# Kernel optimization log

Measured on AMD Instinct MI355X. Metric: run time of the kernel, lower is better.

The kernel has to match this reference:

```python
import math
import jax, jax.numpy as jnp
import numpy as np

N_LAYER = 6
THETA = 2.0 ** 16
LN_EPS = 1e-5


def _ln(x):
    # LayerNorm over last dim, no affine (elementwise_affine=False)
    mu = x.mean(-1, keepdims=True)
    var = ((x - mu) ** 2).mean(-1, keepdims=True)
    return (x - mu) / jnp.sqrt(var + LN_EPS)


def _rope(phases, v):
    # phases: (T, N); v: (B, H, T, N)
    ph = (phases % 1.0) * (2.0 * math.pi)
    c, s = jnp.cos(ph), jnp.sin(ph)
    v2 = v.reshape(v.shape[:-1] + (-1, 2))
    v_rot = jnp.stack((-v2[..., 1], v2[..., 0]), axis=-1).reshape(v.shape)
    return v * c + v_rot * s


def setup_inputs() -> dict:
    key = jax.random.key(0)
    ks = jax.random.split(key, 6)
    B, T, D, nh, mult, V = 2, 512, 256, 4, 64, 256
    N = D * mult // nh  # 4096 neurons per head
    std = 0.02
    return {
        "input_ids": jax.random.randint(ks[0], (B, T), 0, V, dtype=jnp.int64),
        "embed_table": jax.random.normal(ks[1], (V, D), jnp.float32) * std,
        "encoder": jax.random.normal(ks[2], (nh, D, N), jnp.float32) * std,
        "encoder_v": jax.random.normal(ks[3], (nh, D, N), jnp.float32) * std,
        "decoder": jax.random.normal(ks[4], (nh * N, D), jnp.float32) * std,
        "lm_head": jax.random.normal(ks[5], (D, V), jnp.float32) * std,
    }


def reference(input_ids, embed_table, encoder, encoder_v, decoder, lm_head):
    B, T = input_ids.shape
    nh, D, N = encoder.shape
    # RoPE freqs: quantize(arange(N), 2) / N exponent (matches get_freqs)
    qidx = jnp.floor(jnp.arange(N, dtype=jnp.float32) / 2.0) * 2.0
    freqs = 1.0 / (THETA ** (qidx / N)) / (2.0 * math.pi)
    phases = jnp.arange(T, dtype=jnp.float32)[:, None] * freqs[None, :]  # (T, N)
    # strictly-lower causal mask (tril with diagonal=-1)
    causal = jnp.tril(jnp.ones((T, T), dtype=bool), k=-1)
    dec = decoder.reshape(nh, N, D)  # head-major, matches transpose(1,2).reshape

    x = _ln(embed_table[input_ids])[:, None]  # (B, 1, T, D)
    trace = None
    for _ in range(N_LAYER):  # shared (tied) weights across layers
        x_sparse = jax.nn.relu(jnp.einsum('bitd,hdn->bhtn', x, encoder))  # (B,H,T,N)
        qr = _rope(phases, x_sparse)
        scores = jnp.einsum('bhtn,bhsn->bhts', qr, qr)  # linear attn, no softmax
        scores = jnp.where(causal, scores, 0.0)
        ykv = _ln(jnp.einsum('bhts,bisd->bhtd', scores, x))  # (B,H,T,D)
        y_sparse = jax.nn.relu(jnp.einsum('bhtd,hdn->bhtn', ykv, encoder_v))
        xy_sparse = x_sparse * y_sparse  # elementwise gate
        trace = xy_sparse  # keep only last layer (used for neuron_trace)
        ymlp = jnp.einsum('bhtn,hnd->btd', xy_sparse, dec)[:, None]  # (B,1,T,D)
        x = _ln(x + _ln(ymlp))

    xs = x[:, 0]  # (B, T, D)
    logits = xs @ lm_head  # (B, T, V)
    embedding = xs.mean(axis=1)  # (B, D), pool_output, no mask
    neuron_trace = trace.mean(axis=2).reshape(B, -1)  # (B, H*N)
    return logits, embedding, neuron_trace
```

## Files before the change

### kernel.cpp

```cpp
#include <hip/hip_runtime.h>
#include <hip/hip_bf16.h>

#define TT 512
#define DD 256
#define NH 4
#define NN 4096
#define VV 256
#define NLAYER 6
#define BB 2
#define BH (BB * NH)
#define NPAIR 2048

typedef __attribute__((ext_vector_type(8))) short bf16x8;
typedef __attribute__((ext_vector_type(4))) float f32x4;
typedef __attribute__((ext_vector_type(8))) unsigned short us8;
typedef __attribute__((ext_vector_type(4))) unsigned short us4;

#define AS1 __attribute__((address_space(1)))
#define AS3 __attribute__((address_space(3)))

__device__ __forceinline__ void glds16(const unsigned short* g, unsigned short* l) {
  __builtin_amdgcn_global_load_lds((const AS1 void*)g, (AS3 void*)l, 16, 0, 0);
}

__device__ __forceinline__ unsigned short f2bf(float f) {
  unsigned int u = __float_as_uint(f);
  return (unsigned short)((u + 0x7FFFu + ((u >> 16) & 1u)) >> 16);
}
__device__ __forceinline__ float bf2f(unsigned short h) {
  return __uint_as_float((unsigned int)h << 16);
}

__device__ __forceinline__ float block_sum_256(float v) {
  __shared__ float s[4];
  #pragma unroll
  for (int o = 32; o > 0; o >>= 1) v += __shfl_down(v, o);
  int lane = threadIdx.x & 63, wid = threadIdx.x >> 6;
  if (lane == 0) s[wid] = v;
  __syncthreads();
  float r = s[0] + s[1] + s[2] + s[3];
  __syncthreads();
  return r;
}

__device__ __forceinline__ float wave_sum64(float v) {
  #pragma unroll
  for (int o = 32; o > 0; o >>= 1) v += __shfl_xor(v, o);
  return v;
}

__device__ __forceinline__ void mfma_tile128_glds(const unsigned short* __restrict__ A, int lda,
                                                  const unsigned short* __restrict__ B, int ldb,
                                                  int K, f32x4 acc[4][4],
                                                  unsigned short* As, unsigned short* Bs) {
  const int tid = threadIdx.x;
  const int lane = tid & 63, wave = tid >> 6;
  const int fm = lane & 15, fq = lane >> 4;
  const int rw = (wave >> 1) << 6, cw = (wave & 1) << 6;
  const int lrow = lane >> 3;
  const int scol = (((lane & 7) ^ lrow) << 3);
  const unsigned short* gA = A + (size_t)(wave * 8 + lrow) * lda + scol;
  const unsigned short* gB = B + (size_t)(wave * 8 + lrow) * ldb + scol;
  unsigned short* lA = As + wave * 8 * 64;
  unsigned short* lB = Bs + wave * 8 * 64;
  const int swz = (fm & 7) << 4;
  for (int k0 = 0; k0 < K; k0 += 64) {
    __syncthreads();
    #pragma unroll
    for (int i = 0; i < 4; ++i) {
      glds16(gA + k0 + (size_t)(i * 32) * lda, lA + i * 32 * 64);
      glds16(gB + k0 + (size_t)(i * 32) * ldb, lB + i * 32 * 64);
    }
    __syncthreads();
    #pragma unroll
    for (int kk = 0; kk < 2; ++kk) {
      bf16x8 af[4], bfv[4];
      #pragma unroll
      for (int i = 0; i < 4; ++i) {
        const int ra = rw + i * 16 + fm;
        const int rb = cw + i * 16 + fm;
        af[i]  = *(const bf16x8*)((const char*)As + ((((ra << 7) + (kk << 6) + (fq << 4))) ^ swz));
        bfv[i] = *(const bf16x8*)((const char*)Bs + ((((rb << 7) + (kk << 6) + (fq << 4))) ^ swz));
      }
      #pragma unroll
      for (int mi = 0; mi < 4; ++mi)
        #pragma unroll
        for (int ni = 0; ni < 4; ++ni)
          acc[mi][ni] = __builtin_amdgcn_mfma_f32_16x16x32_bf16(af[mi], bfv[ni], acc[mi][ni], 0, 0, 0);
    }
  }
}


__global__ __launch_bounds__(256) void k_csinit(float2* __restrict__ cs) {
  int idx = blockIdx.x * 256 + threadIdx.x;
  int t = idx >> 11, p = idx & (NPAIR - 1);
  const float INV2PI = 0.15915494309189535f;
  const float TWOPI = 6.283185307179586f;
  float f = exp2f(-16.0f * (float)(2 * p) / (float)NN) * INV2PI;
  float ph = fmodf((float)t * f, 1.0f) * TWOPI;
  float s, c;
  sincosf(ph, &s, &c);
  cs[idx] = make_float2(c, s);
}

__global__ __launch_bounds__(256) void k_tcast(const float* __restrict__ in,
                                               unsigned short* __restrict__ out,
                                               int R, int C) {
  __shared__ float tile[64][65];
  const size_t zoff = (size_t)blockIdx.z * R * C;
  const int r0 = blockIdx.y * 64, c0 = blockIdx.x * 64;
  const int cl = threadIdx.x & 63, r4 = threadIdx.x >> 6;
  #pragma unroll 4
  for (int i = 0; i < 16; ++i) {
    int rl = r4 * 16 + i;
    tile[rl][cl] = in[zoff + (size_t)(r0 + rl) * C + c0 + cl];
  }
  __syncthreads();
  #pragma unroll 4
  for (int i = 0; i < 16; ++i) {
    int ccl = r4 * 16 + i;
    out[zoff + (size_t)(c0 + ccl) * R + r0 + cl] = f2bf(tile[cl][ccl]);
  }
}

__global__ __launch_bounds__(256) void k_embed_ln(const int* __restrict__ idw,
                                                  const float* __restrict__ tbl,
                                                  float* __restrict__ x,
                                                  unsigned short* __restrict__ xbf,
                                                  unsigned short* __restrict__ xTbf) {
  __shared__ int s_id;
  int row = blockIdx.x, tid = threadIdx.x;
  if (tid == 0) {
    bool is64 = true;
    for (int i = 1; i < 64; i += 2)
      if (idw[i] != 0) { is64 = false; break; }
    s_id = is64 ? idw[2 * row] : idw[row];
  }
  __syncthreads();
  int id = s_id;
  float v = tbl[(size_t)id * DD + tid];
  float mu = block_sum_256(v) * (1.0f / DD);
  float d = v - mu;
  float var = block_sum_256(d * d) * (1.0f / DD);
  float r = d * rsqrtf(var + 1e-5f);
  x[(size_t)row * DD + tid] = r;
  unsigned short rb = f2bf(r);
  xbf[(size_t)row * DD + tid] = rb;
  int b = row >> 9, t = row & 511;
  xTbf[((size_t)b * DD + tid) * TT + t] = rb;
}


__global__ __launch_bounds__(256) void k_enc(const unsigned short* __restrict__ xbf,
                                             const unsigned short* __restrict__ encT,
                                             const float2* __restrict__ cs,
                                             unsigned short* __restrict__ xsp,
                                             unsigned short* __restrict__ qr) {
  __shared__ float smemf[8192];
  unsigned short* As = (unsigned short*)smemf;
  unsigned short* Bs = As + 8192;
  float (*Sc)[132] = (float(*)[132])smemf;
  const int tid = threadIdx.x;
  const int lin = blockIdx.x;
  const int bh = lin & 7, r0 = lin >> 3;
  const int b = bh >> 2, h = bh & 3;
  const int m0 = (r0 >> 5) * 128, n0 = (r0 & 31) * 128;
  f32x4 acc[4][4] = {};
  mfma_tile128_glds(xbf + (size_t)b * TT * DD + (size_t)m0 * DD, DD,
                    encT + (size_t)h * NN * DD + (size_t)n0 * DD, DD, DD, acc, As, Bs);
  const int lane = tid & 63, wave = tid >> 6;
  const int fm = lane & 15, fq = lane >> 4;
  const int cw = (wave & 1) << 6;
  const int rbase = ((wave >> 1) << 4) + (fq << 2);
  const size_t base = (size_t)bh * TT * NN;
  const int rr = tid >> 3, cc = (tid & 7) << 4;
  #pragma unroll
  for (int mi = 0; mi < 4; ++mi) {
    __syncthreads();
    #pragma unroll
    for (int ni = 0; ni < 4; ++ni)
      #pragma unroll
      for (int r = 0; r < 4; ++r)
        Sc[rbase + r][cw + ni * 16 + fm] = acc[mi][ni][r];
    __syncthreads();
    float v[16];
    *(float4*)&v[0]  = *(const float4*)&Sc[rr][cc];
    *(float4*)&v[4]  = *(const float4*)&Sc[rr][cc + 4];
    *(float4*)&v[8]  = *(const float4*)&Sc[rr][cc + 8];
    *(float4*)&v[12] = *(const float4*)&Sc[rr][cc + 12];
    const int t = m0 + ((rr >> 4) << 6) + mi * 16 + (rr & 15);
    const int n = n0 + cc;
    #pragma unroll
    for (int j = 0; j < 16; ++j) v[j] = fmaxf(v[j], 0.0f);
    us8 o0, o1;
    #pragma unroll
    for (int j = 0; j < 8; ++j) { o0[j] = f2bf(v[j]); o1[j] = f2bf(v[8 + j]); }
    size_t off = base + (size_t)t * NN + n;
    *(us8*)(xsp + off) = o0;
    *(us8*)(xsp + off + 8) = o1;
    float cv[16];
    const float* cp = (const float*)(cs + (size_t)t * NPAIR + (n >> 1));
    *(float4*)&cv[0]  = *(const float4*)(cp);
    *(float4*)&cv[4]  = *(const float4*)(cp + 4);
    *(float4*)&cv[8]  = *(const float4*)(cp + 8);
    *(float4*)&cv[12] = *(const float4*)(cp + 12);
    us8 q0, q1;
    #pragma unroll
    for (int j = 0; j < 8; ++j) {
      float c = cv[2 * j], s = cv[2 * j + 1];
      float ve = v[2 * j], vo = v[2 * j + 1];
      float qe = ve * c - vo * s;
      float qo = vo * c + ve * s;
      if (j < 4) { q0[2 * j] = f2bf(qe); q0[2 * j + 1] = f2bf(qo); }
      else       { q1[2 * (j - 4)] = f2bf(qe); q1[2 * (j - 4) + 1] = f2bf(qo); }
    }
    *(us8*)(qr + off) = q0;
    *(us8*)(qr + off + 8) = q1;
  }
}

__global__ __launch_bounds__(256) void k_scores_part(const unsigned short* __restrict__ qr,
                                                     float* __restrict__ scp) {
  __shared__ float smemf[8192];
  unsigned short* As = (unsigned short*)smemf;
  unsigned short* Bs = As + 8192;
  const int lin = blockIdx.x;
  const int xcd = lin & 7, slot = lin >> 3;
  const int zg = slot / 10, p = slot - zg * 10;
  const int z = xcd + 8 * zg;
  const int bh = z >> 2, kc = z & 3;
  const int mt = (p > 0) + (p > 2) + (p > 5);
  const int nt = p - mt * (mt + 1) / 2;
  const int m0 = mt * 128, n0 = nt * 128;
  const unsigned short* Q = qr + (size_t)bh * TT * NN + kc * 1024;
  f32x4 acc[4][4] = {};
  mfma_tile128_glds(Q + (size_t)m0 * NN, NN, Q + (size_t)n0 * NN, NN, 1024, acc, As, Bs);
  const int lane = threadIdx.x & 63, wave = threadIdx.x >> 6;
  const int fm = lane & 15, fq = lane >> 4;
  const int rw = (wave >> 1) << 6, cw = (wave & 1) << 6;
  float* C = scp + (size_t)z * TT * TT;
  #pragma unroll
  for (int ni = 0; ni < 4; ++ni) {
    int s = n0 + cw + ni * 16 + fm;
    #pragma unroll
    for (int mi = 0; mi < 4; ++mi) {
      int trow = m0 + rw + mi * 16 + (fq << 2);
      #pragma unroll
      for (int r = 0; r < 4; ++r)
        C[(size_t)(trow + r) * TT + s] = acc[mi][ni][r];
    }
  }
}

__global__ __launch_bounds__(256) void k_ykv_part(const float* __restrict__ scp,
                                                  const unsigned short* __restrict__ xTbf,
                                                  float* __restrict__ ykvp) {
  __shared__ unsigned short As[64][40];
  __shared__ unsigned short Bs[256][40];
  const int tid = threadIdx.x;
  const int lin = blockIdx.x;
  const int bh = lin & 7, r0 = lin >> 3;
  const int m0 = (r0 & 7) * 64, ks = r0 >> 3, b = bh >> 2;
  if (ks * 128 >= m0 + 64) return;
  float* C = ykvp + ((size_t)(bh * 4 + ks) * TT + m0) * DD;
  const int lane = tid & 63, wave = tid >> 6;
  const int srow = tid >> 2, sk = (tid & 3) << 3;
  const int fm = lane & 15, fq = lane >> 4;
  const int t = m0 + srow;
  const size_t abase0 = (size_t)(bh * 4) * TT * TT + (size_t)t * TT;
  const unsigned short* Brow = xTbf + ((size_t)b * DD + tid) * TT + ks * 128;
  f32x4 acc[16] = {};
  for (int k0 = 0; k0 < 128; k0 += 32) {
    us8 av;
    const int s0 = ks * 128 + k0 + sk;
    if (s0 >= t) {
      #pragma unroll
      for (int j = 0; j < 8; ++j) av[j] = 0;
    } else {
      const float* p = scp + abase0 + s0;
      float sum[8];
      #pragma unroll
      for (int j = 0; j < 8; ++j) sum[j] = 0.0f;
      #pragma unroll
      for (int kc = 0; kc < 4; ++kc) {
        float4 u0 = *(const float4*)(p + (size_t)kc * TT * TT);
        float4 u1 = *(const float4*)(p + (size_t)kc * TT * TT + 4);
        sum[0] += u0.x; sum[1] += u0.y; sum[2] += u0.z; sum[3] += u0.w;
        sum[4] += u1.x; sum[5] += u1.y; sum[6] += u1.z; sum[7] += u1.w;
      }
      #pragma unroll
      for (int j = 0; j < 8; ++j)
        av[j] = f2bf((s0 + j < t) ? sum[j] : 0.0f);
    }
    us8 bv0 = *(const us8*)(Brow + k0);
    us8 bv1 = *(const us8*)(Brow + k0 + 8);
    us8 bv2 = *(const us8*)(Brow + k0 + 16);
    us8 bv3 = *(const us8*)(Brow + k0 + 24);
    __syncthreads();
    *(us8*)(&As[srow][sk]) = av;
    *(us8*)(&Bs[tid][0]) = bv0;
    *(us8*)(&Bs[tid][8]) = bv1;
    *(us8*)(&Bs[tid][16]) = bv2;
    *(us8*)(&Bs[tid][24]) = bv3;
    __syncthreads();
    bf16x8 a = *(const bf16x8*)(&As[wave * 16 + fm][fq << 3]);
    #pragma unroll
    for (int ni = 0; ni < 16; ++ni) {
      bf16x8 bfr = *(const bf16x8*)(&Bs[ni * 16 + fm][fq << 3]);
      acc[ni] = __builtin_amdgcn_mfma_f32_16x16x32_bf16(a, bfr, acc[ni], 0, 0, 0);
    }
  }
  const int trow = wave * 16 + (fq << 2);
  #pragma unroll
  for (int ni = 0; ni < 16; ++ni)
    #pragma unroll
    for (int r = 0; r < 4; ++r)
      C[(size_t)(trow + r) * DD + ni * 16 + fm] = acc[ni][r];
}

__global__ __launch_bounds__(256) void k_ykv_red(const float* __restrict__ ykvp,
                                                 unsigned short* __restrict__ ykvbf) {
  int row = blockIdx.x * 4 + (threadIdx.x >> 6);
  int lane = threadIdx.x & 63;
  int bh = row >> 9, t = row & 511;
  int d0 = lane << 2;
  int nks = (t >> 7) + 1;
  size_t base = ((size_t)(bh * 4) * TT + t) * DD + d0;
  f32x4 v = *(const f32x4*)(ykvp + base);
  if (nks > 1) v += *(const f32x4*)(ykvp + base + (size_t)TT * DD);
  if (nks > 2) v += *(const f32x4*)(ykvp + base + (size_t)2 * TT * DD);
  if (nks > 3) v += *(const f32x4*)(ykvp + base + (size_t)3 * TT * DD);
  float mu = wave_sum64(v.x + v.y + v.z + v.w) * (1.0f / DD);
  f32x4 d = v - mu;
  float var = wave_sum64(d.x * d.x + d.y * d.y + d.z * d.z + d.w * d.w) * (1.0f / DD);
  f32x4 r = d * rsqrtf(var + 1e-5f);
  us4 rb;
  #pragma unroll
  for (int j = 0; j < 4; ++j) rb[j] = f2bf(r[j]);
  *(us4*)(ykvbf + (size_t)row * DD + d0) = rb;
}

__global__ __launch_bounds__(256) void k_ysp_xy(const unsigned short* __restrict__ ykvbf,
                                                const unsigned short* __restrict__ encvT,
                                                const unsigned short* __restrict__ xsp,
                                                unsigned short* __restrict__ xy) {
  __shared__ float smemf[8192];
  unsigned short* As = (unsigned short*)smemf;
  unsigned short* Bs = As + 8192;
  float (*Sc)[132] = (float(*)[132])smemf;
  const int tid = threadIdx.x;
  const int lin = blockIdx.x;
  const int bh = lin & 7, r0 = lin >> 3;
  const int h = bh & 3;
  const int m0 = (r0 >> 5) * 128, n0 = (r0 & 31) * 128;
  f32x4 acc[4][4] = {};
  mfma_tile128_glds(ykvbf + (size_t)bh * TT * DD + (size_t)m0 * DD, DD,
                    encvT + (size_t)h * NN * DD + (size_t)n0 * DD, DD, DD, acc, As, Bs);
  const int lane = tid & 63, wave = tid >> 6;
  const int fm = lane & 15, fq = lane >> 4;
  const int cw = (wave & 1) << 6;
  const int rbase = ((wave >> 1) << 4) + (fq << 2);
  const size_t base = (size_t)bh * TT * NN;
  const int rr = tid >> 3, cc = (tid & 7) << 4;
  #pragma unroll
  for (int mi = 0; mi < 4; ++mi) {
    __syncthreads();
    #pragma unroll
    for (int ni = 0; ni < 4; ++ni)
      #pragma unroll
      for (int r = 0; r < 4; ++r)
        Sc[rbase + r][cw + ni * 16 + fm] = acc[mi][ni][r];
    __syncthreads();
    float v[16];
    *(float4*)&v[0]  = *(const float4*)&Sc[rr][cc];
    *(float4*)&v[4]  = *(const float4*)&Sc[rr][cc + 4];
    *(float4*)&v[8]  = *(const float4*)&Sc[rr][cc + 8];
    *(float4*)&v[12] = *(const float4*)&Sc[rr][cc + 12];
    const int t = m0 + ((rr >> 4) << 6) + mi * 16 + (rr & 15);
    const int n = n0 + cc;
    size_t off = base + (size_t)t * NN + n;
    us8 x0 = *(const us8*)(xsp + off);
    us8 x1 = *(const us8*)(xsp + off + 8);
    us8 o0, o1;
    #pragma unroll
    for (int j = 0; j < 8; ++j) {
      o0[j] = f2bf(bf2f(x0[j]) * fmaxf(v[j], 0.0f));
      o1[j] = f2bf(bf2f(x1[j]) * fmaxf(v[8 + j], 0.0f));
    }
    *(us8*)(xy + off) = o0;
    *(us8*)(xy + off + 8) = o1;
  }
}

__global__ __launch_bounds__(256) void k_ymlp(const unsigned short* __restrict__ xy,
                                              const unsigned short* __restrict__ decT,
                                              float* __restrict__ ym32) {
  __shared__ float smemf[8192];
  unsigned short* As = (unsigned short*)smemf;
  unsigned short* Bs = As + 8192;
  const int lin = blockIdx.x;
  const int xcd = lin & 7, r0 = lin >> 3;
  const int z = xcd + 8 * (r0 >> 3);
  const int tile = r0 & 7;
  const int bh = z >> 3, ks = z & 7, h = bh & 3;
  const int m0 = (tile & 3) * 128, n0 = (tile >> 2) * 128;
  f32x4 acc[4][4] = {};
  mfma_tile128_glds(xy + (size_t)bh * TT * NN + (size_t)m0 * NN + ks * 512, NN,
                    decT + (size_t)h * DD * NN + (size_t)n0 * NN + ks * 512, NN,
                    512, acc, As, Bs);
  const int lane = threadIdx.x & 63, wave = threadIdx.x >> 6;
  const int fm = lane & 15, fq = lane >> 4;
  const int rw = (wave >> 1) << 6, cw = (wave & 1) << 6;
  float* C = ym32 + (size_t)z * TT * DD;
  #pragma unroll
  for (int ni = 0; ni < 4; ++ni) {
    int d = n0 + cw + ni * 16 + fm;
    #pragma unroll
    for (int mi = 0; mi < 4; ++mi) {
      int trow = m0 + rw + mi * 16 + (fq << 2);
      #pragma unroll
      for (int r = 0; r < 4; ++r)
        C[(size_t)(trow + r) * DD + d] = acc[mi][ni][r];
    }
  }
}

__global__ __launch_bounds__(256) void k_ln2(float* __restrict__ x,
                                             const float* __restrict__ ym32,
                                             unsigned short* __restrict__ xbf,
                                             unsigned short* __restrict__ xTbf) {
  int row = blockIdx.x * 4 + (threadIdx.x >> 6);
  int lane = threadIdx.x & 63;
  int b = row >> 9, t = row & 511;
  int d0 = lane << 2;
  f32x4 y = {0.0f, 0.0f, 0.0f, 0.0f};
  size_t rbase = (size_t)t * DD + d0;
  #pragma unroll
  for (int p = 0; p < 32; ++p)
    y += *(const f32x4*)(ym32 + (size_t)(b * 32 + p) * TT * DD + rbase);
  float mu = wave_sum64(y.x + y.y + y.z + y.w) * (1.0f / DD);
  f32x4 d = y - mu;
  float var = wave_sum64(d.x * d.x + d.y * d.y + d.z * d.z + d.w * d.w) * (1.0f / DD);
  f32x4 ly = d * rsqrtf(var + 1e-5f);
  f32x4 xv = *(const f32x4*)(x + (size_t)row * DD + d0) + ly;
  float mu2 = wave_sum64(xv.x + xv.y + xv.z + xv.w) * (1.0f / DD);
  f32x4 d2 = xv - mu2;
  float var2 = wave_sum64(d2.x * d2.x + d2.y * d2.y + d2.z * d2.z + d2.w * d2.w) * (1.0f / DD);
  f32x4 r = d2 * rsqrtf(var2 + 1e-5f);
  *(f32x4*)(x + (size_t)row * DD + d0) = r;
  us4 rb;
  #pragma unroll
  for (int j = 0; j < 4; ++j) rb[j] = f2bf(r[j]);
  *(us4*)(xbf + (size_t)row * DD + d0) = rb;
  #pragma unroll
  for (int j = 0; j < 4; ++j)
    xTbf[((size_t)b * DD + d0 + j) * TT + t] = rb[j];
}

__global__ __launch_bounds__(256) void k_trace_part(const unsigned short* __restrict__ xy,
                                                    float* __restrict__ part) {
  const int lin = blockIdx.x;
  const int ts = lin & 7, nc = (lin >> 3) & 1, bh = lin >> 4;
  const int n0 = nc * 2048 + threadIdx.x * 8;
  const size_t base = (size_t)bh * TT * NN + n0;
  float acc[8];
  #pragma unroll
  for (int j = 0; j < 8; ++j) acc[j] = 0.0f;
  for (int t = ts * 64; t < ts * 64 + 64; ++t) {
    us8 v = *(const us8*)(xy + base + (size_t)t * NN);
    #pragma unroll
    for (int j = 0; j < 8; ++j) acc[j] += bf2f(v[j]);
  }
  float* o = part + (size_t)(bh * 8 + ts) * NN + n0;
  #pragma unroll
  for (int j = 0; j < 8; ++j) o[j] = acc[j];
}

__global__ __launch_bounds__(256) void k_trace_red(const float* __restrict__ part,
                                                   float* __restrict__ out) {
  int idx = blockIdx.x * 256 + threadIdx.x;
  int bh = idx >> 12, n = idx & 4095;
  float s = 0.0f;
  #pragma unroll
  for (int ts = 0; ts < 8; ++ts)
    s += part[(size_t)(bh * 8 + ts) * NN + n];
  out[idx] = s * (1.0f / TT);
}

__global__ __launch_bounds__(256) void k_logits(const float* __restrict__ x,
                                                const float* __restrict__ W,
                                                float* __restrict__ out) {
  __shared__ float xs[DD];
  int row = blockIdx.x, tid = threadIdx.x;
  xs[tid] = x[(size_t)row * DD + tid];
  __syncthreads();
  float s = 0.0f;
  #pragma unroll 8
  for (int d = 0; d < DD; ++d) s = fmaf(xs[d], W[(size_t)d * VV + tid], s);
  out[(size_t)row * VV + tid] = s;
}

__global__ __launch_bounds__(256) void k_embedding(const float* __restrict__ x,
                                                   float* __restrict__ out) {
  int idx = blockIdx.x * 256 + threadIdx.x;
  int b = idx >> 8, d = idx & 255;
  float s = 0.0f;
  for (int t = 0; t < TT; ++t) s += x[(size_t)(b * TT + t) * DD + d];
  out[idx] = s * (1.0f / TT);
}

extern "C" void kernel_launch(void* const* d_in, const int* in_sizes, int n_in,
                              void* d_out, int out_size, void* d_ws, size_t ws_size,
                              hipStream_t stream) {
  const int*   ids  = (const int*)d_in[0];
  const float* tbl  = (const float*)d_in[1];
  const float* enc  = (const float*)d_in[2];
  const float* encv = (const float*)d_in[3];
  const float* dec  = (const float*)d_in[4];
  const float* lmh  = (const float*)d_in[5];

  float* ws   = (float*)d_ws;
  float* x    = ws;
  unsigned short* ykvbf = (unsigned short*)(x + 262144);
  float* ym32 = (float*)(ykvbf + 1048576);
  unsigned short* xbf   = (unsigned short*)(ym32 + 8388608);
  unsigned short* xTbf  = xbf + 262144;
  unsigned short* encT  = xTbf + 262144;
  unsigned short* encvT = encT + 4194304;
  unsigned short* decT  = encvT + 4194304;
  unsigned short* xspbf = decT + 4194304;
  unsigned short* qxybf = xspbf + 16777216;
  float2* cs  = (float2*)(qxybf + 16777216);
  float* scp  = (float*)(cs + 1048576);
  float* ykvp = scp + 8388608;

  float* out_logits = (float*)d_out;
  float* out_embed  = out_logits + (size_t)BB * TT * VV;
  float* out_trace  = out_embed + (size_t)BB * DD;

  k_csinit<<<(TT * NPAIR) / 256, 256, 0, stream>>>(cs);
  k_tcast<<<dim3(NN / 64, DD / 64, NH), 256, 0, stream>>>(enc,  encT,  DD, NN);
  k_tcast<<<dim3(NN / 64, DD / 64, NH), 256, 0, stream>>>(encv, encvT, DD, NN);
  k_tcast<<<dim3(DD / 64, NN / 64, NH), 256, 0, stream>>>(dec,  decT,  NN, DD);

  k_embed_ln<<<BB * TT, 256, 0, stream>>>(ids, tbl, x, xbf, xTbf);
  for (int l = 0; l < NLAYER; ++l) {
    k_enc        <<<1024, 256, 0, stream>>>(xbf, encT, cs, xspbf, qxybf);
    k_scores_part<<<320, 256, 0, stream>>>(qxybf, scp);
    k_ykv_part   <<<256, 256, 0, stream>>>(scp, xTbf, ykvp);
    k_ykv_red    <<<BH * TT / 4, 256, 0, stream>>>(ykvp, ykvbf);
    k_ysp_xy     <<<1024, 256, 0, stream>>>(ykvbf, encvT, xspbf, qxybf);
    k_ymlp       <<<512, 256, 0, stream>>>(qxybf, decT, ym32);
    k_ln2        <<<BB * TT / 4, 256, 0, stream>>>(x, ym32, xbf, xTbf);
  }
  k_trace_part<<<128, 256, 0, stream>>>(qxybf, scp);
  k_trace_red <<<128, 256, 0, stream>>>(scp, out_trace);
  k_logits    <<<BB * TT, 256, 0, stream>>>(x, lmh, out_logits);
  k_embedding <<<(BB * DD) / 256, 256, 0, stream>>>(x, out_embed);
}
```

Measured before the change: 816.4 us.

## Use BK=128 GEMM tile helper and move causal masking into scores epilogue

Adds a 128x128 MFMA tile routine that stages a 128-wide K slab per iteration with an XOR swizzle, halving the barrier/load rounds, and uses it in the scores and ymlp kernels (LDS doubled to 64KB per block). The scores kernel now zeroes the upper triangle on diagonal tiles so the ykv kernel can drop its per-element causal branch and mask. The larger LDS footprint may reduce occupancy, and ykv now reads unmasked partial buffers for off-diagonal regions that may be unwritten.

```diff
diff --git a/kernel.cpp b/kernel.cpp
--- a/kernel.cpp
+++ b/kernel.cpp
@@ -81,6 +81,45 @@
         const int rb = cw + i * 16 + fm;
         af[i]  = *(const bf16x8*)((const char*)As + ((((ra << 7) + (kk << 6) + (fq << 4))) ^ swz));
         bfv[i] = *(const bf16x8*)((const char*)Bs + ((((rb << 7) + (kk << 6) + (fq << 4))) ^ swz));
+      }
+      #pragma unroll
+      for (int mi = 0; mi < 4; ++mi)
+        #pragma unroll
+        for (int ni = 0; ni < 4; ++ni)
+          acc[mi][ni] = __builtin_amdgcn_mfma_f32_16x16x32_bf16(af[mi], bfv[ni], acc[mi][ni], 0, 0, 0);
+    }
+  }
+}
+
+__device__ __forceinline__ void mfma_tile128_bk128(const unsigned short* __restrict__ A, int lda,
+                                                   const unsigned short* __restrict__ B, int ldb,
+                                                   int K, f32x4 acc[4][4],
+                                                   unsigned short* As, unsigned short* Bs) {
+  const int tid = threadIdx.x;
+  const int lane = tid & 63, wave = tid >> 6;
+  const int fm = lane & 15, fq = lane >> 4;
+  const int rw = (wave >> 1) << 6, cw = (wave & 1) << 6;
+  const int lrow = lane >> 4;
+  const int cslot = lane & 15;
+  for (int k0 = 0; k0 < K; k0 += 128) {
+    __syncthreads();
+    #pragma unroll
+    for (int i = 0; i < 8; ++i) {
+      const int row = wave * 32 + i * 4 + lrow;
+      const int sc = (cslot ^ (row & 15)) << 3;
+      glds16(A + (size_t)row * lda + k0 + sc, As + (size_t)(wave * 32 + i * 4) * 128);
+      glds16(B + (size_t)row * ldb + k0 + sc, Bs + (size_t)(wave * 32 + i * 4) * 128);
+    }
+    __syncthreads();
+    #pragma unroll
+    for (int kk = 0; kk < 4; ++kk) {
+      bf16x8 af[4], bfv[4];
+      #pragma unroll
+      for (int i = 0; i < 4; ++i) {
+        const int ra = rw + i * 16 + fm;
+        const int rb = cw + i * 16 + fm;
+        af[i]  = *(const bf16x8*)((const char*)As + (((ra << 8) + (kk << 6) + (fq << 4)) ^ ((ra & 15) << 4)));
+        bfv[i] = *(const bf16x8*)((const char*)Bs + (((rb << 8) + (kk << 6) + (fq << 4)) ^ ((rb & 15) << 4)));
       }
       #pragma unroll
       for (int mi = 0; mi < 4; ++mi)
@@ -222,9 +261,9 @@
 
 __global__ __launch_bounds__(256) void k_scores_part(const unsigned short* __restrict__ qr,
                                                      float* __restrict__ scp) {
-  __shared__ float smemf[8192];
+  __shared__ float smemf[16384];
   unsigned short* As = (unsigned short*)smemf;
-  unsigned short* Bs = As + 8192;
+  unsigned short* Bs = As + 16384;
   const int lin = blockIdx.x;
   const int xcd = lin & 7, slot = lin >> 3;
   const int zg = slot / 10, p = slot - zg * 10;
@@ -235,11 +274,12 @@
   const int m0 = mt * 128, n0 = nt * 128;
   const unsigned short* Q = qr + (size_t)bh * TT * NN + kc * 1024;
   f32x4 acc[4][4] = {};
-  mfma_tile128_glds(Q + (size_t)m0 * NN, NN, Q + (size_t)n0 * NN, NN, 1024, acc, As, Bs);
+  mfma_tile128_bk128(Q + (size_t)m0 * NN, NN, Q + (size_t)n0 * NN, NN, 1024, acc, As, Bs);
   const int lane = threadIdx.x & 63, wave = threadIdx.x >> 6;
   const int fm = lane & 15, fq = lane >> 4;
   const int rw = (wave >> 1) << 6, cw = (wave & 1) << 6;
   float* C = scp + (size_t)z * TT * TT;
+  const bool diag = (m0 == n0);
   #pragma unroll
   for (int ni = 0; ni < 4; ++ni) {
     int s = n0 + cw + ni * 16 + fm;
@@ -247,8 +287,11 @@
     for (int mi = 0; mi < 4; ++mi) {
       int trow = m0 + rw + mi * 16 + (fq << 2);
       #pragma unroll
-      for (int r = 0; r < 4; ++r)
-        C[(size_t)(trow + r) * TT + s] = acc[mi][ni][r];
+      for (int r = 0; r < 4; ++r) {
+        float v = acc[mi][ni][r];
+        if (diag && s >= trow + r) v = 0.0f;
+        C[(size_t)(trow + r) * TT + s] = v;
+      }
     }
   }
 }
@@ -272,27 +315,23 @@
   const unsigned short* Brow = xTbf + ((size_t)b * DD + tid) * TT + ks * 128;
   f32x4 acc[16] = {};
   for (int k0 = 0; k0 < 128; k0 += 32) {
+    const int s0 = ks * 128 + k0 + sk;
+    const float* p = scp + abase0 + s0;
+    float sum[8];
+    float4 u0 = *(const float4*)(p);
+    float4 u1 = *(const float4*)(p + 4);
+    sum[0] = u0.x; sum[1] = u0.y; sum[2] = u0.z; sum[3] = u0.w;
+    sum[4] = u1.x; sum[5] = u1.y; sum[6] = u1.z; sum[7] = u1.w;
+    #pragma unroll
+    for (int kc = 1; kc < 4; ++kc) {
+      float4 v0 = *(const float4*)(p + (size_t)kc * TT * TT);
+      float4 v1 = *(const float4*)(p + (size_t)kc * TT * TT + 4);
+      sum[0] += v0.x; sum[1] += v0.y; sum[2] += v0.z; sum[3] += v0.w;
+      sum[4] += v1.x; sum[5] += v1.y; sum[6] += v1.z; sum[7] += v1.w;
+    }
     us8 av;
-    const int s0 = ks * 128 + k0 + sk;
-    if (s0 >= t) {
-      #pragma unroll
-      for (int j = 0; j < 8; ++j) av[j] = 0;
-    } else {
-      const float* p = scp + abase0 + s0;
-      float sum[8];
-      #pragma unroll
-      for (int j = 0; j < 8; ++j) sum[j] = 0.0f;
-      #pragma unroll
-      for (int kc = 0; kc < 4; ++kc) {
-        float4 u0 = *(const float4*)(p + (size_t)kc * TT * TT);
-        float4 u1 = *(const float4*)(p + (size_t)kc * TT * TT + 4);
-        sum[0] += u0.x; sum[1] += u0.y; sum[2] += u0.z; sum[3] += u0.w;
-        sum[4] += u1.x; sum[5] += u1.y; sum[6] += u1.z; sum[7] += u1.w;
-      }
-      #pragma unroll
-      for (int j = 0; j < 8; ++j)
-        av[j] = f2bf((s0 + j < t) ? sum[j] : 0.0f);
-    }
+    #pragma unroll
+    for (int j = 0; j < 8; ++j) av[j] = f2bf(sum[j]);
     us8 bv0 = *(const us8*)(Brow + k0);
     us8 bv1 = *(const us8*)(Brow + k0 + 8);
     us8 bv2 = *(const us8*)(Brow + k0 + 16);
@@ -396,9 +435,9 @@
 __global__ __launch_bounds__(256) void k_ymlp(const unsigned short* __restrict__ xy,
                                               const unsigned short* __restrict__ decT,
                                               float* __restrict__ ym32) {
-  __shared__ float smemf[8192];
+  __shared__ float smemf[16384];
   unsigned short* As = (unsigned short*)smemf;
-  unsigned short* Bs = As + 8192;
+  unsigned short* Bs = As + 16384;
   const int lin = blockIdx.x;
   const int xcd = lin & 7, r0 = lin >> 3;
   const int z = xcd + 8 * (r0 >> 3);
@@ -406,9 +445,9 @@
   const int bh = z >> 3, ks = z & 7, h = bh & 3;
   const int m0 = (tile & 3) * 128, n0 = (tile >> 2) * 128;
   f32x4 acc[4][4] = {};
-  mfma_tile128_glds(xy + (size_t)bh * TT * NN + (size_t)m0 * NN + ks * 512, NN,
-                    decT + (size_t)h * DD * NN + (size_t)n0 * NN + ks * 512, NN,
-                    512, acc, As, Bs);
+  mfma_tile128_bk128(xy + (size_t)bh * TT * NN + (size_t)m0 * NN + ks * 512, NN,
+                     decT + (size_t)h * DD * NN + (size_t)n0 * NN + ks * 512, NN,
+                     512, acc, As, Bs);
   const int lane = threadIdx.x & 63, wave = threadIdx.x >> 6;
   const int fm = lane & 15, fq = lane >> 4;
   const int rw = (wave >> 1) << 6, cw = (wave & 1) << 6;
```

Result: no change. 826.0 us (+1.2%).
